# Optimization experiments

Hardware: AMD Instinct MI355X
Metric: run time of the kernel (lower is better)

The kernel has to match this reference:

```python
import jax, jax.numpy as jnp
import numpy as np

H = 768
R = 7  # len(DISCOURSE_RELATIONS)


def setup_inputs() -> dict:
    key = jax.random.key(0)
    ks = jax.random.split(key, 6)
    B, S = 4, 256
    scale = 1.0 / np.sqrt(H)
    return {
        "pooled_outputs": jax.random.normal(ks[0], (B, S, H), dtype=jnp.float32),
        "w_src": jax.random.uniform(ks[1], (H, H), jnp.float32, -scale, scale),
        "b_src": jax.random.uniform(ks[2], (H,), jnp.float32, -scale, scale),
        "w_tgt": jax.random.uniform(ks[3], (H, H), jnp.float32, -scale, scale),
        "b_tgt": jax.random.uniform(ks[4], (H,), jnp.float32, -scale, scale),
        "w_out": jax.random.uniform(ks[5], (R, H), jnp.float32, -scale, scale),
    }


def reference(pooled_outputs, w_src, b_src, w_tgt, b_tgt, w_out):
    # h_src, h_tgt: [B, S, H]
    h_src = jnp.einsum("bsh,kh->bsk", pooled_outputs, w_src) + b_src
    h_tgt = jnp.einsum("bth,kh->btk", pooled_outputs, w_tgt) + b_tgt
    # broadcast add -> [B, S, S, H], tanh, then small-output linear -> [B, S, S, R]
    h = jnp.tanh(h_src[:, :, None, :] + h_tgt[:, None, :, :])
    return jnp.einsum("bsth,rh->bstr", h, w_out)
```

## Files before the change

kernel.cpp:

```cpp
#include <hip/hip_runtime.h>
#include <hip/hip_bf16.h>

#define HD 768
#define SQ 256
#define NB 4
#define RR 7

typedef short bf16x8 __attribute__((ext_vector_type(8)));
typedef float f32x4  __attribute__((ext_vector_type(4)));

__device__ __forceinline__ float fast_tanh(float x) {
  float e = __expf(2.0f * x);
  return 1.0f - 2.0f / (e + 1.0f);
}

__device__ __forceinline__ float pair_tanh(float a, float b) {
  return (a + b) * __builtin_amdgcn_rcpf(fmaf(a, b, 1.0f));
}

__device__ __forceinline__ short f2bf(float x) {
  return (short)__builtin_bit_cast(unsigned short, __float2bfloat16(x));
}

__device__ __forceinline__ void gl_lds16(const void* g, void* l) {
  __builtin_amdgcn_global_load_lds(
      (const __attribute__((address_space(1))) void*)g,
      (__attribute__((address_space(3))) void*)l, 16, 0, 0);
}

__global__ __launch_bounds__(256) void cvt_kernel(
    const float* __restrict__ X, const float* __restrict__ Ws,
    const float* __restrict__ Wt,
    short* __restrict__ Xb, short* __restrict__ Wsb, short* __restrict__ Wtb)
{
  const int NX = NB * SQ * HD / 8;
  const int NW = HD * HD / 8;
  int i = blockIdx.x * 256 + threadIdx.x;
  const float* src; short* dst;
  if (i < NX)               { src = X;  dst = Xb; }
  else if (i < NX + NW)     { src = Ws; dst = Wsb; i -= NX; }
  else if (i < NX + 2 * NW) { src = Wt; dst = Wtb; i -= NX + NW; }
  else return;
  float4 a = *(const float4*)(src + (size_t)i * 8);
  float4 b = *(const float4*)(src + (size_t)i * 8 + 4);
  bf16x8 r;
  r[0] = f2bf(a.x); r[1] = f2bf(a.y); r[2] = f2bf(a.z); r[3] = f2bf(a.w);
  r[4] = f2bf(b.x); r[5] = f2bf(b.y); r[6] = f2bf(b.z); r[7] = f2bf(b.w);
  *(bf16x8*)(dst + (size_t)i * 8) = r;
}

__global__ __launch_bounds__(256) void stage1_lds(
    const short* __restrict__ Xb,
    const short* __restrict__ Wsb, const float* __restrict__ bsrc,
    const short* __restrict__ Wtb, const float* __restrict__ btgt,
    float* __restrict__ ta, float* __restrict__ tb)
{
  constexpr int BK = 64;
  const short* W  = blockIdx.z ? Wtb : Wsb;
  const float* bv = blockIdx.z ? btgt : bsrc;
  float* outp     = blockIdx.z ? tb : ta;
  const int row0 = blockIdx.x * 64, col0 = blockIdx.y * 64;

  __shared__ short As[64 * BK];
  __shared__ short Bs[64 * BK];

  const int tid = threadIdx.x, wave = tid >> 6, lane = tid & 63;
  const int wm = (wave >> 1) * 32, wn = (wave & 1) * 32;

  f32x4 acc[2][2] = {};

  const int G0 = wave * 64 + lane;
  const int r0 = G0 >> 3, g0 = G0 & 7;
  const int G1 = G0 + 256;
  const int r1 = G1 >> 3, g1 = G1 & 7;

  for (int k0 = 0; k0 < HD; k0 += BK) {
    __syncthreads();
    gl_lds16(Xb + (size_t)(row0 + r0) * HD + k0 + ((g0 ^ (r0 & 7)) * 8),
             As + (size_t)(wave * 64) * 8);
    gl_lds16(Xb + (size_t)(row0 + r1) * HD + k0 + ((g1 ^ (r1 & 7)) * 8),
             As + (size_t)(256 + wave * 64) * 8);
    gl_lds16(W + (size_t)(col0 + r0) * HD + k0 + ((g0 ^ (r0 & 7)) * 8),
             Bs + (size_t)(wave * 64) * 8);
    gl_lds16(W + (size_t)(col0 + r1) * HD + k0 + ((g1 ^ (r1 & 7)) * 8),
             Bs + (size_t)(256 + wave * 64) * 8);
    __syncthreads();

    #pragma unroll
    for (int kkb = 0; kkb < 2; ++kkb) {
      bf16x8 af[2], bw[2];
      const int q = kkb * 4 + (lane >> 4);
      #pragma unroll
      for (int i = 0; i < 2; ++i) {
        int ar = wm + i * 16 + (lane & 15);
        af[i] = *(const bf16x8*)&As[ar * BK + ((q ^ (ar & 7)) * 8)];
        int br = wn + i * 16 + (lane & 15);
        bw[i] = *(const bf16x8*)&Bs[br * BK + ((q ^ (br & 7)) * 8)];
      }
      #pragma unroll
      for (int i = 0; i < 2; ++i)
        #pragma unroll
        for (int j = 0; j < 2; ++j)
          acc[i][j] = __builtin_amdgcn_mfma_f32_16x16x32_bf16(af[i], bw[j], acc[i][j], 0, 0, 0);
    }
  }

  #pragma unroll
  for (int j = 0; j < 2; ++j) {
    int n = col0 + wn + j * 16 + (lane & 15);
    float bb = bv[n];
    #pragma unroll
    for (int i = 0; i < 2; ++i)
      #pragma unroll
      for (int r = 0; r < 4; ++r) {
        int m = row0 + wm + i * 16 + (lane >> 4) * 4 + r;
        outp[(size_t)m * HD + n] = fast_tanh(acc[i][j][r] + bb);
      }
  }
}

__global__ __launch_bounds__(256) void stage1_mfma(
    const float* __restrict__ X,
    const float* __restrict__ Wsrc, const float* __restrict__ bsrc,
    const float* __restrict__ Wtgt, const float* __restrict__ btgt,
    float* __restrict__ ta, float* __restrict__ tb)
{
  constexpr int BK = 64;
  const float* W  = blockIdx.z ? Wtgt : Wsrc;
  const float* bv = blockIdx.z ? btgt : bsrc;
  float* outp     = blockIdx.z ? tb : ta;
  const int row0 = blockIdx.x * 64, col0 = blockIdx.y * 64;

  __shared__ short As[64 * BK];
  __shared__ short Bs[64 * BK];

  const int tid  = threadIdx.x;
  const int wave = tid >> 6, lane = tid & 63;
  const int wm = (wave >> 1) * 32, wn = (wave & 1) * 32;
  f32x4 acc[2][2] = {};
  const int sr = tid >> 2, sq = tid & 3;

  for (int k0 = 0; k0 < HD; k0 += BK) {
    const float* xa = X + (size_t)(row0 + sr) * HD + k0 + sq * 16;
    const float* xw = W + (size_t)(col0 + sr) * HD + k0 + sq * 16;
    float4 a0 = *(const float4*)(xa + 0), a1 = *(const float4*)(xa + 4);
    float4 a2 = *(const float4*)(xa + 8), a3 = *(const float4*)(xa + 12);
    float4 w0 = *(const float4*)(xw + 0), w1 = *(const float4*)(xw + 4);
    float4 w2 = *(const float4*)(xw + 8), w3 = *(const float4*)(xw + 12);
    __syncthreads();
    bf16x8 p;
    p[0]=f2bf(a0.x);p[1]=f2bf(a0.y);p[2]=f2bf(a0.z);p[3]=f2bf(a0.w);
    p[4]=f2bf(a1.x);p[5]=f2bf(a1.y);p[6]=f2bf(a1.z);p[7]=f2bf(a1.w);
    *(bf16x8*)&As[sr * BK + (((sq * 2 + 0) ^ (sr & 7)) * 8)] = p;
    p[0]=f2bf(a2.x);p[1]=f2bf(a2.y);p[2]=f2bf(a2.z);p[3]=f2bf(a2.w);
    p[4]=f2bf(a3.x);p[5]=f2bf(a3.y);p[6]=f2bf(a3.z);p[7]=f2bf(a3.w);
    *(bf16x8*)&As[sr * BK + (((sq * 2 + 1) ^ (sr & 7)) * 8)] = p;
    p[0]=f2bf(w0.x);p[1]=f2bf(w0.y);p[2]=f2bf(w0.z);p[3]=f2bf(w0.w);
    p[4]=f2bf(w1.x);p[5]=f2bf(w1.y);p[6]=f2bf(w1.z);p[7]=f2bf(w1.w);
    *(bf16x8*)&Bs[sr * BK + (((sq * 2 + 0) ^ (sr & 7)) * 8)] = p;
    p[0]=f2bf(w2.x);p[1]=f2bf(w2.y);p[2]=f2bf(w2.z);p[3]=f2bf(w2.w);
    p[4]=f2bf(w3.x);p[5]=f2bf(w3.y);p[6]=f2bf(w3.z);p[7]=f2bf(w3.w);
    *(bf16x8*)&Bs[sr * BK + (((sq * 2 + 1) ^ (sr & 7)) * 8)] = p;
    __syncthreads();

    #pragma unroll
    for (int kkb = 0; kkb < 2; ++kkb) {
      bf16x8 af[2], bw[2];
      const int q = kkb * 4 + (lane >> 4);
      #pragma unroll
      for (int i = 0; i < 2; ++i) {
        int ar = wm + i * 16 + (lane & 15);
        af[i] = *(const bf16x8*)&As[ar * BK + ((q ^ (ar & 7)) * 8)];
        int br = wn + i * 16 + (lane & 15);
        bw[i] = *(const bf16x8*)&Bs[br * BK + ((q ^ (br & 7)) * 8)];
      }
      #pragma unroll
      for (int i = 0; i < 2; ++i)
        #pragma unroll
        for (int j = 0; j < 2; ++j)
          acc[i][j] = __builtin_amdgcn_mfma_f32_16x16x32_bf16(af[i], bw[j], acc[i][j], 0, 0, 0);
    }
  }

  #pragma unroll
  for (int j = 0; j < 2; ++j) {
    int n = col0 + wn + j * 16 + (lane & 15);
    float bb = bv[n];
    #pragma unroll
    for (int i = 0; i < 2; ++i)
      #pragma unroll
      for (int r = 0; r < 4; ++r) {
        int m = row0 + wm + i * 16 + (lane >> 4) * 4 + r;
        outp[(size_t)m * HD + n] = fast_tanh(acc[i][j][r] + bb);
      }
  }
}

__global__ __launch_bounds__(256, 4) void stage2_mfma(
    const float* __restrict__ ta, const float* __restrict__ tb,
    const float* __restrict__ Wout, float* __restrict__ out)
{
  constexpr int HC = 128, LDp = 132;
  const int b  = blockIdx.z;
  const int s0 = blockIdx.y * 16, t0 = blockIdx.x * 16;

  __shared__ float sa[16][LDp];
  __shared__ float sb[16][LDp];
  __shared__ f32x4 red[4][4][64];

  const int tid = threadIdx.x, wave = tid >> 6, lane = tid & 63;
  const int lg = lane >> 4;
  const int ln = lane & 15;
  const int kh = wave & 1;
  const int sh = wave >> 1;
  const int kb = kh * 64;

  f32x4 acc[8] = {};

  const float* taB = ta + ((size_t)b * SQ + s0) * HD;
  const float* tbB = tb + ((size_t)b * SQ + t0) * HD;

  for (int c = 0; c < HD / HC; ++c) {
    __syncthreads();
    #pragma unroll
    for (int j = 0; j < 2; ++j) {
      int idx = tid + 256 * j, r = idx >> 5, q = idx & 31;
      *(float4*)&sa[r][q * 4] = *(const float4*)(taB + (size_t)r * HD + c * HC + q * 4);
      *(float4*)&sb[r][q * 4] = *(const float4*)(tbB + (size_t)r * HD + c * HC + q * 4);
    }
    __syncthreads();

    #pragma unroll
    for (int m = 0; m < 2; ++m) {
      const int kk = kb + m * 32 + lg * 8;
      bf16x8 bfr;
      float4 u = {0.f,0.f,0.f,0.f}, v = {0.f,0.f,0.f,0.f};
      if (ln < RR) {
        const float* wp = Wout + (size_t)ln * HD + c * HC + kk;
        u = *(const float4*)wp; v = *(const float4*)(wp + 4);
      }
      bfr[0]=f2bf(u.x); bfr[1]=f2bf(u.y); bfr[2]=f2bf(u.z); bfr[3]=f2bf(u.w);
      bfr[4]=f2bf(v.x); bfr[5]=f2bf(v.y); bfr[6]=f2bf(v.z); bfr[7]=f2bf(v.w);
      float4 q0 = *(const float4*)&sb[ln][kk];
      float4 q1 = *(const float4*)&sb[ln][kk + 4];
      float bvv[8] = {q0.x,q0.y,q0.z,q0.w,q1.x,q1.y,q1.z,q1.w};

      #pragma unroll
      for (int si = 0; si < 8; ++si) {
        const float* ap = &sa[sh * 8 + si][kk];
        float4 a0 = *(const float4*)ap;
        float4 a1 = *(const float4*)(ap + 4);
        float av[8] = {a0.x,a0.y,a0.z,a0.w,a1.x,a1.y,a1.z,a1.w};
        bf16x8 pa;
        #pragma unroll
        for (int j = 0; j < 8; ++j)
          pa[j] = f2bf(pair_tanh(av[j], bvv[j]));
        acc[si] = __builtin_amdgcn_mfma_f32_16x16x32_bf16(pa, bfr, acc[si], 0, 0, 0);
      }
    }
  }

  #pragma unroll
  for (int sg = 0; sg < 2; ++sg) {
    __syncthreads();
    #pragma unroll
    for (int i = 0; i < 4; ++i)
      red[wave][i][lane] = acc[sg * 4 + i];
    __syncthreads();
    #pragma unroll
    for (int shf = 0; shf < 2; ++shf) {
      f32x4 sum = red[shf * 2 + 0][wave][lane] + red[shf * 2 + 1][wave][lane];
      if (ln < RR) {
        int s = s0 + shf * 8 + sg * 4 + wave;
        float* op = out + (((size_t)b * SQ + s) * SQ + t0 + lg * 4) * RR + ln;
        op[0] = sum[0]; op[RR] = sum[1]; op[2 * RR] = sum[2]; op[3 * RR] = sum[3];
      }
    }
  }
}

extern "C" void kernel_launch(void* const* d_in, const int* in_sizes, int n_in,
                              void* d_out, int out_size, void* d_ws, size_t ws_size,
                              hipStream_t stream) {
  (void)in_sizes; (void)n_in; (void)out_size;
  const float* X    = (const float*)d_in[0];
  const float* Wsrc = (const float*)d_in[1];
  const float* bsrc = (const float*)d_in[2];
  const float* Wtgt = (const float*)d_in[3];
  const float* btgt = (const float*)d_in[4];
  const float* Wout = (const float*)d_in[5];
  float* out = (float*)d_out;

  float* taF = (float*)d_ws;
  float* tbF = taF + (size_t)NB * SQ * HD;
  const size_t base = (size_t)2 * NB * SQ * HD * sizeof(float);
  const size_t need = base + ((size_t)NB * SQ * HD + 2 * (size_t)HD * HD) * sizeof(short);

  if (ws_size >= need) {
    short* Xb  = (short*)((char*)d_ws + base);
    short* Wsb = Xb + (size_t)NB * SQ * HD;
    short* Wtb = Wsb + (size_t)HD * HD;
    cvt_kernel<<<960, 256, 0, stream>>>(X, Wsrc, Wtgt, Xb, Wsb, Wtb);
    stage1_lds<<<dim3(16, 12, 2), 256, 0, stream>>>(Xb, Wsb, bsrc, Wtb, btgt, taF, tbF);
  } else {
    stage1_mfma<<<dim3(16, 12, 2), 256, 0, stream>>>(X, Wsrc, bsrc, Wtgt, btgt, taF, tbF);
  }
  stage2_mfma<<<dim3(SQ / 16, SQ / 16, NB), 256, 0, stream>>>(taF, tbF, Wout, out);
}
```

Measured before the change: 117.4 us.

## Double-buffer stage1 LDS loads and drop stage2 cross-wave K-split reduction

Result: slower. 120.8 us (+2.9%).

```diff
diff --git a/kernel.cpp b/kernel.cpp
--- a/kernel.cpp
+++ b/kernel.cpp
@@ -61,8 +61,8 @@
   float* outp     = blockIdx.z ? tb : ta;
   const int row0 = blockIdx.x * 64, col0 = blockIdx.y * 64;
 
-  __shared__ short As[64 * BK];
-  __shared__ short Bs[64 * BK];
+  __shared__ short As[2][64 * BK];
+  __shared__ short Bs[2][64 * BK];
 
   const int tid = threadIdx.x, wave = tid >> 6, lane = tid & 63;
   const int wm = (wave >> 1) * 32, wn = (wave & 1) * 32;
@@ -74,17 +74,33 @@
   const int G1 = G0 + 256;
   const int r1 = G1 >> 3, g1 = G1 & 7;
 
+  const size_t xo0 = (size_t)(row0 + r0) * HD + ((g0 ^ (r0 & 7)) * 8);
+  const size_t xo1 = (size_t)(row0 + r1) * HD + ((g1 ^ (r1 & 7)) * 8);
+  const size_t wo0 = (size_t)(col0 + r0) * HD + ((g0 ^ (r0 & 7)) * 8);
+  const size_t wo1 = (size_t)(col0 + r1) * HD + ((g1 ^ (r1 & 7)) * 8);
+  short* const la0 = (short*)As + (size_t)(wave * 64) * 8;
+  short* const la1 = (short*)As + (size_t)(256 + wave * 64) * 8;
+  short* const lb0 = (short*)Bs + (size_t)(wave * 64) * 8;
+  short* const lb1 = (short*)Bs + (size_t)(256 + wave * 64) * 8;
+  constexpr int BUF = 64 * BK;
+
+  gl_lds16(Xb + xo0, la0);
+  gl_lds16(Xb + xo1, la1);
+  gl_lds16(W + wo0, lb0);
+  gl_lds16(W + wo1, lb1);
+
+  int cur = 0;
   for (int k0 = 0; k0 < HD; k0 += BK) {
     __syncthreads();
-    gl_lds16(Xb + (size_t)(row0 + r0) * HD + k0 + ((g0 ^ (r0 & 7)) * 8),
-             As + (size_t)(wave * 64) * 8);
-    gl_lds16(Xb + (size_t)(row0 + r1) * HD + k0 + ((g1 ^ (r1 & 7)) * 8),
-             As + (size_t)(256 + wave * 64) * 8);
-    gl_lds16(W + (size_t)(col0 + r0) * HD + k0 + ((g0 ^ (r0 & 7)) * 8),
-             Bs + (size_t)(wave * 64) * 8);
-    gl_lds16(W + (size_t)(col0 + r1) * HD + k0 + ((g1 ^ (r1 & 7)) * 8),
-             Bs + (size_t)(256 + wave * 64) * 8);
-    __syncthreads();
+    if (k0 + BK < HD) {
+      int nb = (cur ^ 1) * BUF;
+      gl_lds16(Xb + xo0 + k0 + BK, la0 + nb);
+      gl_lds16(Xb + xo1 + k0 + BK, la1 + nb);
+      gl_lds16(W + wo0 + k0 + BK, lb0 + nb);
+      gl_lds16(W + wo1 + k0 + BK, lb1 + nb);
+    }
+    const short* Ac = (const short*)As + cur * BUF;
+    const short* Bc = (const short*)Bs + cur * BUF;
 
     #pragma unroll
     for (int kkb = 0; kkb < 2; ++kkb) {
@@ -93,9 +109,9 @@
       #pragma unroll
       for (int i = 0; i < 2; ++i) {
         int ar = wm + i * 16 + (lane & 15);
-        af[i] = *(const bf16x8*)&As[ar * BK + ((q ^ (ar & 7)) * 8)];
+        af[i] = *(const bf16x8*)&Ac[ar * BK + ((q ^ (ar & 7)) * 8)];
         int br = wn + i * 16 + (lane & 15);
-        bw[i] = *(const bf16x8*)&Bs[br * BK + ((q ^ (br & 7)) * 8)];
+        bw[i] = *(const bf16x8*)&Bc[br * BK + ((q ^ (br & 7)) * 8)];
       }
       #pragma unroll
       for (int i = 0; i < 2; ++i)
@@ -103,6 +119,7 @@
         for (int j = 0; j < 2; ++j)
           acc[i][j] = __builtin_amdgcn_mfma_f32_16x16x32_bf16(af[i], bw[j], acc[i][j], 0, 0, 0);
     }
+    cur ^= 1;
   }
 
   #pragma unroll
@@ -196,7 +213,7 @@
   }
 }
 
-__global__ __launch_bounds__(256, 4) void stage2_mfma(
+__global__ __launch_bounds__(256, 6) void stage2_mfma(
     const float* __restrict__ ta, const float* __restrict__ tb,
     const float* __restrict__ Wout, float* __restrict__ out)
 {
@@ -206,16 +223,12 @@
 
   __shared__ float sa[16][LDp];
   __shared__ float sb[16][LDp];
-  __shared__ f32x4 red[4][4][64];
 
   const int tid = threadIdx.x, wave = tid >> 6, lane = tid & 63;
   const int lg = lane >> 4;
   const int ln = lane & 15;
-  const int kh = wave & 1;
-  const int sh = wave >> 1;
-  const int kb = kh * 64;
-
-  f32x4 acc[8] = {};
+
+  f32x4 acc[4] = {};
 
   const float* taB = ta + ((size_t)b * SQ + s0) * HD;
   const float* tbB = tb + ((size_t)b * SQ + t0) * HD;
@@ -231,10 +244,10 @@
     __syncthreads();
 
     #pragma unroll
-    for (int m = 0; m < 2; ++m) {
-      const int kk = kb + m * 32 + lg * 8;
+    for (int m = 0; m < 4; ++m) {
+      const int kk = m * 32 + lg * 8;
       bf16x8 bfr;
-      float4 u = {0.f,0.f,0.f,0.f}, v = {0.f,0.f,0.f,0.f};
+      float4 u = {0.f, 0.f, 0.f, 0.f}, v = {0.f, 0.f, 0.f, 0.f};
       if (ln < RR) {
         const float* wp = Wout + (size_t)ln * HD + c * HC + kk;
         u = *(const float4*)wp; v = *(const float4*)(wp + 4);
@@ -246,8 +259,8 @@
       float bvv[8] = {q0.x,q0.y,q0.z,q0.w,q1.x,q1.y,q1.z,q1.w};
 
       #pragma unroll
-      for (int si = 0; si < 8; ++si) {
-        const float* ap = &sa[sh * 8 + si][kk];
+      for (int si = 0; si < 4; ++si) {
+        const float* ap = &sa[wave * 4 + si][kk];
         float4 a0 = *(const float4*)ap;
         float4 a1 = *(const float4*)(ap + 4);
         float av[8] = {a0.x,a0.y,a0.z,a0.w,a1.x,a1.y,a1.z,a1.w};
@@ -260,21 +273,15 @@
     }
   }
 
-  #pragma unroll
-  for (int sg = 0; sg < 2; ++sg) {
-    __syncthreads();
-    #pragma unroll
-    for (int i = 0; i < 4; ++i)
-      red[wave][i][lane] = acc[sg * 4 + i];
-    __syncthreads();
-    #pragma unroll
-    for (int shf = 0; shf < 2; ++shf) {
-      f32x4 sum = red[shf * 2 + 0][wave][lane] + red[shf * 2 + 1][wave][lane];
-      if (ln < RR) {
-        int s = s0 + shf * 8 + sg * 4 + wave;
-        float* op = out + (((size_t)b * SQ + s) * SQ + t0 + lg * 4) * RR + ln;
-        op[0] = sum[0]; op[RR] = sum[1]; op[2 * RR] = sum[2]; op[3 * RR] = sum[3];
-      }
+  if (ln < RR) {
+    #pragma unroll
+    for (int si = 0; si < 4; ++si) {
+      int s = s0 + wave * 4 + si;
+      float* op = out + (((size_t)b * SQ + s) * SQ + t0 + lg * 4) * RR + ln;
+      op[0]      = acc[si][0];
+      op[RR]     = acc[si][1];
+      op[2 * RR] = acc[si][2];
+      op[3 * RR] = acc[si][3];
     }
   }
 }
```
